# Kernel optimization log

Measured on AMD Instinct MI355X. Metric: run time of the kernel, lower is better.

The kernel has to match this reference:

```python
import jax, jax.numpy as jnp
from jax import lax
import numpy as np


def setup_inputs() -> dict:
    key = jax.random.key(0)
    ks = jax.random.split(key, 8)
    B, Cin, H, W = 4, 64, 128, 128
    D, N = 2 * Cin, 64  # D = in_ch*2, N = ssd_state_dim*2
    s = np.float32(1.0 / np.sqrt(D))
    return {
        "x": jax.random.normal(ks[0], (B, Cin, H, W), jnp.float32),
        "h_prev": jnp.zeros((B, D, N), jnp.float32),
        "norm_w": jnp.ones((D,), jnp.float32),
        "norm_b": jnp.zeros((D,), jnp.float32),
        "W_x": jax.random.normal(ks[1], (D, D), jnp.float32) * s,
        "W_B": jax.random.normal(ks[2], (N, D), jnp.float32) * s,
        "W_C": jax.random.normal(ks[3], (N, D), jnp.float32) * s,
        "w_dt": jax.random.normal(ks[4], (D,), jnp.float32) * s,
        "dt_bias": jnp.float32(0.0),
        "A_log": jnp.float32(0.0),
        "D_skip": jax.random.normal(ks[5], (D,), jnp.float32),
        "W_out": jax.random.normal(ks[6], (D, D), jnp.float32) * s,
    }


def _forward(x, h_prev, norm_w, norm_b, W_x, W_B, W_C, w_dt, dt_bias, A_log, D_skip, W_out):
    B, C, H, W = x.shape
    # rfft2 -> complex [B, C, Hf, Wf]
    xf = jnp.fft.rfft2(x, norm='ortho')
    Hf, Wf = xf.shape[-2], xf.shape[-1]
    L = Hf * Wf
    sqrt_n = jnp.sqrt(jnp.float32(H * W))
    # pack real/imag along channels: [B, 2C, L]
    u = jnp.concatenate([xf.real.reshape(B, C, L), xf.imag.reshape(B, C, L)], axis=1)
    # LayerNorm1D over the channel dim
    mu = jnp.mean(u, axis=1, keepdims=True)
    var = jnp.var(u, axis=1, keepdims=True)
    u = (u - mu) * lax.rsqrt(var + 1e-5) * norm_w[None, :, None] + norm_b[None, :, None]
    u = u / sqrt_n
    # SSD (Mamba2-style) recurrence over the L frequency tokens
    xs = jnp.einsum('ed,bdl->lbe', W_x, u)   # [L, B, D]
    Bs = jnp.einsum('nd,bdl->lbn', W_B, u)   # [L, B, N]
    Cs = jnp.einsum('nd,bdl->lbn', W_C, u)   # [L, B, N]
    dt = jax.nn.softplus(jnp.einsum('d,bdl->lb', w_dt, u) + dt_bias)  # [L, B]
    dec = jnp.exp(-jnp.exp(A_log) * dt)       # [L, B], A = -exp(A_log)

    def step(h, inp):
        x_t, B_t, C_t, dec_t, dt_t = inp
        h = dec_t[:, None, None] * h + (dt_t[:, None] * x_t)[:, :, None] * B_t[:, None, :]
        y_t = jnp.einsum('bdn,bn->bd', h, C_t)
        return h, y_t

    h_last, ys = lax.scan(step, h_prev, (xs, Bs, Cs, dec, dt))  # ys [L, B, D]
    y = ys.transpose(1, 2, 0) + D_skip[None, :, None] * xs.transpose(1, 2, 0)  # [B, D, L]
    freq_out = jnp.einsum('ed,bdl->bel', W_out, y) * sqrt_n
    # unpack real/imag halves and inverse FFT
    ft = (freq_out[:, :C] + 1j * freq_out[:, C:]).reshape(B, C, Hf, Wf)
    y_sp = jnp.fft.irfft2(ft, s=(H, W), norm='ortho')
    return y_sp, h_last


def reference(x, h_prev, norm_w, norm_b, W_x, W_B, W_C, w_dt, dt_bias, A_log, D_skip, W_out):
    return _forward(x, h_prev, norm_w, norm_b, W_x, W_B, W_C, w_dt, dt_bias, A_log, D_skip, W_out)
```

## Files before the change

kernel.cpp:

```cpp
#include <hip/hip_runtime.h>
#include <hip/hip_bf16.h>
#include <math.h>

#define BB 4
#define CC 64
#define HH 128
#define WW 128
#define DD 128
#define NN 64
#define HF 128
#define WF 65
#define LL 8320
#define TSEG 64
#define NSEG 130
#define PI2f 6.283185307179586f

__device__ __forceinline__ int brev7(int x) { return (int)(__brev((unsigned)x) >> 25); }

__global__ void k0_transpose(const float* __restrict__ Wx, const float* __restrict__ Wb,
                             const float* __restrict__ Wc, const float* __restrict__ Wout,
                             float* __restrict__ WcatT, float* __restrict__ WoT) {
  int idx = blockIdx.x * 256 + threadIdx.x;
  if (idx < 128 * 256) {
    int k = idx >> 8, o = idx & 255;
    float v;
    if (o < 128)      v = Wx[o * 128 + k];
    else if (o < 192) v = Wb[(o - 128) * 128 + k];
    else              v = Wc[(o - 192) * 128 + k];
    WcatT[k * 256 + o] = v;
  }
  if (idx < 128 * 128) {
    int d = idx >> 7, e = idx & 127;
    WoT[d * 128 + e] = Wout[e * 128 + d];
  }
}

__global__ __launch_bounds__(256) void k1_rfft(const float* __restrict__ x,
                                               float* __restrict__ T1) {
  __shared__ float2 data[128 * 17];
  __shared__ float2 tw[64];
  int tid = threadIdx.x;
  if (tid < 64) {
    float sv, cv;
    sincosf(PI2f * (float)tid * (1.f / 128.f), &sv, &cv);
    tw[tid] = make_float2(cv, sv);
  }
  int r0 = blockIdx.x * 32;
  const float* xp = x + (size_t)r0 * 128;
#pragma unroll
  for (int i = 0; i < 8; i++) {
    int e = i * 256 + tid;
    int p = e >> 7, j = e & 127;
    float v1 = xp[(2 * p) * 128 + j];
    float v2 = xp[(2 * p + 1) * 128 + j];
    data[brev7(j) * 17 + p] = make_float2(v1, v2);
  }
  __syncthreads();
  for (int s = 1; s <= 7; s++) {
    int half = 1 << (s - 1);
    int tsh = 7 - s;
#pragma unroll
    for (int i = 0; i < 4; i++) {
      int idx = i * 256 + tid;
      int t = idx >> 4, c = idx & 15;
      int j = t & (half - 1);
      int pos = ((t >> (s - 1)) << s) + j;
      float2 a = data[pos * 17 + c];
      float2 b = data[(pos + half) * 17 + c];
      float2 w = tw[j << tsh];
      float2 m = make_float2(b.x * w.x + b.y * w.y, b.y * w.x - b.x * w.y);
      data[pos * 17 + c] = make_float2(a.x + m.x, a.y + m.y);
      data[(pos + half) * 17 + c] = make_float2(a.x - m.x, a.y - m.y);
    }
    __syncthreads();
  }
  const float inv = 1.f / 128.f;
  float2* o = (float2*)T1 + (size_t)r0 * 65;
#pragma unroll
  for (int i = 0; i < 5; i++) {
    int e = i * 256 + tid;
    if (e < 1040) {
      int p = e / 65, k = e - p * 65;
      float2 Z = data[k * 17 + p];
      float2 Zc = data[((128 - k) & 127) * 17 + p];
      float2 X1 = make_float2((Z.x + Zc.x) * 0.5f * inv, (Z.y - Zc.y) * 0.5f * inv);
      float2 X2 = make_float2((Z.y + Zc.y) * 0.5f * inv, (Zc.x - Z.x) * 0.5f * inv);
      o[(2 * p) * 65 + k] = X1;
      o[(2 * p + 1) * 65 + k] = X2;
    }
  }
}

__global__ __launch_bounds__(256) void k2a_fft(const float* __restrict__ T1,
                                               float* __restrict__ uT) {
  __shared__ float2 data[128 * 34];
  __shared__ float2 tw[64];
  int tid = threadIdx.x;
  if (tid < 64) {
    float sv, cv;
    sincosf(PI2f * (float)tid * (1.f / 128.f), &sv, &cv);
    tw[tid] = make_float2(cv, sv);
  }
  int chunk = blockIdx.x & 1;
  int bc = blockIdx.x >> 1;
  int wf0 = chunk * 32;
  const float2* Tp = (const float2*)T1 + (size_t)bc * 8320;
#pragma unroll
  for (int i = 0; i < 17; i++) {
    int e = i * 256 + tid;
    if (e < 4224) {
      int j = e / 33;
      int c = e - j * 33;
      data[brev7(j) * 34 + c] = Tp[j * 65 + wf0 + c];
    }
  }
  __syncthreads();
  for (int s = 1; s <= 7; s++) {
    int half = 1 << (s - 1);
    int tsh = 7 - s;
#pragma unroll
    for (int i = 0; i < 9; i++) {
      int idx = i * 256 + tid;
      if (idx < 2112) {
        int t = idx / 33;
        int c = idx - t * 33;
        int j = t & (half - 1);
        int pos = ((t >> (s - 1)) << s) + j;
        float2 a = data[pos * 34 + c];
        float2 b = data[(pos + half) * 34 + c];
        float2 w = tw[j << tsh];
        float2 m = make_float2(b.x * w.x + b.y * w.y, b.y * w.x - b.x * w.y);
        data[pos * 34 + c] = make_float2(a.x + m.x, a.y + m.y);
        data[(pos + half) * 34 + c] = make_float2(a.x - m.x, a.y - m.y);
      }
    }
    __syncthreads();
  }
  int b = bc >> 6, ch = bc & 63;
  float* pr = uT + (size_t)(b * 128 + ch) * 8320;
  float* pi = uT + (size_t)(b * 128 + 64 + ch) * 8320;
#pragma unroll
  for (int i = 0; i < 17; i++) {
    int e = i * 256 + tid;
    if (e < 4224) {
      int hf = e / 33;
      int c = e - hf * 33;
      float2 v = data[hf * 34 + c];
      pr[hf * 65 + wf0 + c] = v.x;
      pi[hf * 65 + wf0 + c] = v.y;
    }
  }
}

__global__ __launch_bounds__(512) void k3_ln_proj(
    const float* __restrict__ uT, const float* __restrict__ WcatT,
    const float* __restrict__ nw, const float* __restrict__ nb,
    const float* __restrict__ wdt, const float* __restrict__ dtbias,
    float* __restrict__ xs, float* __restrict__ Bs, float* __restrict__ Cs,
    float* __restrict__ dtb) {
  __shared__ float su[128 * 68];
  __shared__ float snw[128], snb[128], swdt[128];
  int tid = threadIdx.x;
  int b = blockIdx.x / 130, tile = blockIdx.x % 130;
  int l0 = tile * 64;
  if (tid < 128) { snw[tid] = nw[tid]; snb[tid] = nb[tid]; swdt[tid] = wdt[tid]; }
  const float* up = uT + (size_t)b * 128 * 8320 + l0;
#pragma unroll
  for (int i = 0; i < 4; i++) {
    int e = i * 512 + tid;
    int d = e >> 4, q = e & 15;
    float4 v = *(const float4*)(up + (size_t)d * 8320 + q * 4);
    *(float4*)&su[d * 68 + q * 4] = v;
  }
  __syncthreads();
  int t = tid >> 3, j = tid & 7;
  float vals[16];
  float s = 0.f, s2 = 0.f;
#pragma unroll
  for (int i = 0; i < 16; i++) {
    float v = su[(8 * i + j) * 68 + t];
    vals[i] = v; s += v; s2 += v * v;
  }
  s += __shfl_xor(s, 1, 64);  s += __shfl_xor(s, 2, 64);  s += __shfl_xor(s, 4, 64);
  s2 += __shfl_xor(s2, 1, 64); s2 += __shfl_xor(s2, 2, 64); s2 += __shfl_xor(s2, 4, 64);
  float mu = s * (1.f / 128.f);
  float var = s2 * (1.f / 128.f) - mu * mu;
  float rs = rsqrtf(var + 1e-5f);
  float raw = 0.f;
#pragma unroll
  for (int i = 0; i < 16; i++) {
    int k = 8 * i + j;
    float v = ((vals[i] - mu) * rs * snw[k] + snb[k]) * (1.f / 128.f);
    su[k * 68 + t] = v;
    raw = fmaf(v, swdt[k], raw);
  }
  raw += __shfl_xor(raw, 1, 64); raw += __shfl_xor(raw, 2, 64); raw += __shfl_xor(raw, 4, 64);
  if (j == 0) {
    float z = raw + dtbias[0];
    float sp = fmaxf(z, 0.f) + log1pf(expf(-fabsf(z)));
    dtb[b * LL + l0 + t] = sp;
  }
  __syncthreads();
  int wv = tid >> 6;
  int lane = tid & 63;
  int t0 = wv * 8;
  float acc[8][4];
#pragma unroll
  for (int i = 0; i < 8; i++)
#pragma unroll
    for (int r = 0; r < 4; r++) acc[i][r] = 0.f;
  const float4* W4 = (const float4*)WcatT;
  for (int k = 0; k < 128; k++) {
    float4 w = W4[k * 64 + lane];
    const float4* sr4 = (const float4*)&su[k * 68 + t0];
    float4 u0 = sr4[0], u1 = sr4[1];
    float uk[8] = {u0.x, u0.y, u0.z, u0.w, u1.x, u1.y, u1.z, u1.w};
#pragma unroll
    for (int i = 0; i < 8; i++) {
      acc[i][0] = fmaf(w.x, uk[i], acc[i][0]);
      acc[i][1] = fmaf(w.y, uk[i], acc[i][1]);
      acc[i][2] = fmaf(w.z, uk[i], acc[i][2]);
      acc[i][3] = fmaf(w.w, uk[i], acc[i][3]);
    }
  }
  size_t tok0 = (size_t)b * LL + l0 + t0;
  float* basep;
  size_t stride;
  if (lane < 32)      { basep = xs + tok0 * 128 + lane * 4;        stride = 128; }
  else if (lane < 48) { basep = Bs + tok0 * 64 + (lane - 32) * 4;  stride = 64; }
  else                { basep = Cs + tok0 * 64 + (lane - 48) * 4;  stride = 64; }
#pragma unroll
  for (int i = 0; i < 8; i++)
    *(float4*)(basep + (size_t)i * stride) =
        make_float4(acc[i][0], acc[i][1], acc[i][2], acc[i][3]);
}

__global__ __launch_bounds__(256) void k5_seg(
    const float* __restrict__ xs, const float* __restrict__ Bs, const float* __restrict__ Cs,
    const float* __restrict__ dtb, const float* __restrict__ Alog,
    const float* __restrict__ Dskip,
    float* __restrict__ ybuf, float* __restrict__ Sseg, float* __restrict__ ssegb,
    float* __restrict__ cumg) {
  __shared__ __align__(16) float sX[64 * 68];
  __shared__ __align__(16) float sB[64 * 68];
  __shared__ __align__(16) float sCM[64 * 68];
  __shared__ float sdt[64], slc[64], sws[64];
  int tid = threadIdx.x;
  int half = blockIdx.x & 1;
  int bs = blockIdx.x >> 1;
  int b = bs / NSEG, seg = bs % NSEG;
  int tokbase = b * LL + seg * TSEG;
  const float4* xg = (const float4*)(xs + (size_t)tokbase * 128);
#pragma unroll
  for (int i = 0; i < 4; i++) {
    int e = i * 256 + tid;
    int t = e >> 4, q = e & 15;
    *(float4*)&sX[t * 68 + q * 4] = xg[t * 32 + half * 16 + q];
  }
  const float4* bg = (const float4*)(Bs + (size_t)tokbase * 64);
  const float4* cg = (const float4*)(Cs + (size_t)tokbase * 64);
#pragma unroll
  for (int i = 0; i < 4; i++) {
    int e = i * 256 + tid;
    int t = e >> 4, n4 = e & 15;
    *(float4*)&sB[t * 68 + n4 * 4] = bg[e];
    *(float4*)&sCM[t * 68 + n4 * 4] = cg[e];
  }
  if (tid < 64) sdt[tid] = dtb[tokbase + tid];
  __syncthreads();
  if (tid < 64) {
    float a = expf(Alog[0]);
    float v = -a * sdt[tid];
#pragma unroll
    for (int off = 1; off < 64; off <<= 1) {
      float o = __shfl_up(v, off, 64);
      if (tid >= off) v += o;
    }
    slc[tid] = v;
    float l63 = __shfl(v, 63, 64);
    sws[tid] = expf(l63 - v) * sdt[tid];
    if (half == 0) {
      cumg[tokbase + tid] = expf(v);
      if (tid == 63) ssegb[seg * BB + b] = expf(v);
    }
  }
  __syncthreads();
  int t0 = (tid >> 4) * 4, s0 = (tid & 15) * 4;
  float g[4][4];
#pragma unroll
  for (int i = 0; i < 4; i++)
#pragma unroll
    for (int j = 0; j < 4; j++) g[i][j] = 0.f;
  for (int n4 = 0; n4 < 16; n4++) {
    float4 cr[4], br[4];
#pragma unroll
    for (int i = 0; i < 4; i++) cr[i] = *(const float4*)&sCM[(t0 + i) * 68 + n4 * 4];
#pragma unroll
    for (int j = 0; j < 4; j++) br[j] = *(const float4*)&sB[(s0 + j) * 68 + n4 * 4];
#pragma unroll
    for (int i = 0; i < 4; i++)
#pragma unroll
      for (int j = 0; j < 4; j++) {
        g[i][j] = fmaf(cr[i].x, br[j].x, g[i][j]);
        g[i][j] = fmaf(cr[i].y, br[j].y, g[i][j]);
        g[i][j] = fmaf(cr[i].z, br[j].z, g[i][j]);
        g[i][j] = fmaf(cr[i].w, br[j].w, g[i][j]);
      }
  }
  __syncthreads();
#pragma unroll
  for (int i = 0; i < 4; i++) {
    int t = t0 + i;
    float4 m;
    float lt = slc[t];
    m.x = (s0 + 0 <= t) ? expf(lt - slc[s0 + 0]) * sdt[s0 + 0] * g[i][0] : 0.f;
    m.y = (s0 + 1 <= t) ? expf(lt - slc[s0 + 1]) * sdt[s0 + 1] * g[i][1] : 0.f;
    m.z = (s0 + 2 <= t) ? expf(lt - slc[s0 + 2]) * sdt[s0 + 2] * g[i][2] : 0.f;
    m.w = (s0 + 3 <= t) ? expf(lt - slc[s0 + 3]) * sdt[s0 + 3] * g[i][3] : 0.f;
    *(float4*)&sCM[t * 68 + s0] = m;
  }
  __syncthreads();
  {
    int d0 = (tid & 15) * 4;
    float acc[4][4];
#pragma unroll
    for (int i = 0; i < 4; i++)
#pragma unroll
      for (int j = 0; j < 4; j++) acc[i][j] = 0.f;
    for (int s = 0; s < 64; s++) {
      float4 xv = *(const float4*)&sX[s * 68 + d0];
#pragma unroll
      for (int i = 0; i < 4; i++) {
        float m = sCM[(t0 + i) * 68 + s];
        acc[i][0] = fmaf(m, xv.x, acc[i][0]);
        acc[i][1] = fmaf(m, xv.y, acc[i][1]);
        acc[i][2] = fmaf(m, xv.z, acc[i][2]);
        acc[i][3] = fmaf(m, xv.w, acc[i][3]);
      }
    }
    float4 dk = *(const float4*)&Dskip[half * 64 + d0];
#pragma unroll
    for (int i = 0; i < 4; i++) {
      int t = t0 + i;
      float4 xv = *(const float4*)&sX[t * 68 + d0];
      float4 y;
      y.x = fmaf(dk.x, xv.x, acc[i][0]);
      y.y = fmaf(dk.y, xv.y, acc[i][1]);
      y.z = fmaf(dk.z, xv.z, acc[i][2]);
      y.w = fmaf(dk.w, xv.w, acc[i][3]);
      *(float4*)(ybuf + (size_t)(tokbase + t) * 128 + half * 64 + d0) = y;
    }
  }
  {
    int dd0 = (tid >> 4) * 4, n0 = (tid & 15) * 4;
    float sacc[4][4];
#pragma unroll
    for (int k = 0; k < 4; k++)
#pragma unroll
      for (int j = 0; j < 4; j++) sacc[k][j] = 0.f;
    for (int s = 0; s < 64; s++) {
      float w = sws[s];
      float4 b4 = *(const float4*)&sB[s * 68 + n0];
      b4.x *= w; b4.y *= w; b4.z *= w; b4.w *= w;
      float4 xv = *(const float4*)&sX[s * 68 + dd0];
      float xk[4] = {xv.x, xv.y, xv.z, xv.w};
#pragma unroll
      for (int k = 0; k < 4; k++) {
        sacc[k][0] = fmaf(xk[k], b4.x, sacc[k][0]);
        sacc[k][1] = fmaf(xk[k], b4.y, sacc[k][1]);
        sacc[k][2] = fmaf(xk[k], b4.z, sacc[k][2]);
        sacc[k][3] = fmaf(xk[k], b4.w, sacc[k][3]);
      }
    }
    float* Sp = Sseg + (size_t)seg * 32768 + (size_t)b * 8192;
#pragma unroll
    for (int k = 0; k < 4; k++)
      *(float4*)&Sp[(half * 64 + dd0 + k) * 64 + n0] =
          make_float4(sacc[k][0], sacc[k][1], sacc[k][2], sacc[k][3]);
  }
}

__global__ void k5b_states(const float* __restrict__ h_prev, const float* __restrict__ Sseg,
                           const float* __restrict__ ssegb, float* __restrict__ Hp,
                           float* __restrict__ h_last) {
  int gid = blockIdx.x * 256 + threadIdx.x;
  int b = gid >> 13;
  float h = h_prev[gid];
  for (int p = 0; p < NSEG; p++) {
    Hp[(size_t)p * 32768 + gid] = h;
    h = fmaf(ssegb[p * 4 + b], h, Sseg[(size_t)p * 32768 + gid]);
  }
  h_last[gid] = h;
}

__global__ __launch_bounds__(512) void k5c_correct(
    const float* __restrict__ Cs, const float* __restrict__ Hp,
    const float* __restrict__ cumg, float* __restrict__ ybuf) {
  __shared__ __align__(16) float Ct[64 * 64];
  __shared__ __align__(16) float Ht[64 * 132];
  __shared__ float cg[64];
  int tid = threadIdx.x;
  int b = blockIdx.x / NSEG, seg = blockIdx.x % NSEG;
  int tokbase = b * LL + seg * 64;
  const float* Csrc = Cs + (size_t)tokbase * 64;
#pragma unroll
  for (int i = 0; i < 8; i++) {
    int e = tid + i * 512;
    Ct[(e & 63) * 64 + (e >> 6)] = Csrc[e];
  }
  const float* Hsrc = Hp + (size_t)seg * 32768 + (size_t)b * 8192;
#pragma unroll
  for (int i = 0; i < 16; i++) {
    int e = tid + i * 512;
    Ht[(e & 63) * 132 + (e >> 6)] = Hsrc[e];
  }
  if (tid < 64) cg[tid] = cumg[tokbase + tid];
  __syncthreads();
  int og = tid & 15, tg = tid >> 4;
  int d0 = og * 8, t0 = tg * 2;
  float acc[2][8];
#pragma unroll
  for (int i = 0; i < 2; i++)
#pragma unroll
    for (int jj = 0; jj < 8; jj++) acc[i][jj] = 0.f;
  for (int n = 0; n < 64; n++) {
    float2 c2 = *(const float2*)&Ct[n * 64 + t0];
    float4 h0 = *(const float4*)&Ht[n * 132 + d0];
    float4 h1 = *(const float4*)&Ht[n * 132 + d0 + 4];
    float cv[2] = {c2.x, c2.y};
    float hv[8] = {h0.x, h0.y, h0.z, h0.w, h1.x, h1.y, h1.z, h1.w};
#pragma unroll
    for (int i = 0; i < 2; i++)
#pragma unroll
      for (int jj = 0; jj < 8; jj++) acc[i][jj] = fmaf(cv[i], hv[jj], acc[i][jj]);
  }
#pragma unroll
  for (int i = 0; i < 2; i++) {
    float sc = cg[t0 + i];
    float* yp = ybuf + (size_t)(tokbase + t0 + i) * 128 + d0;
    float4 y0 = *(float4*)yp;
    float4 y1 = *(float4*)(yp + 4);
    y0.x = fmaf(sc, acc[i][0], y0.x); y0.y = fmaf(sc, acc[i][1], y0.y);
    y0.z = fmaf(sc, acc[i][2], y0.z); y0.w = fmaf(sc, acc[i][3], y0.w);
    y1.x = fmaf(sc, acc[i][4], y1.x); y1.y = fmaf(sc, acc[i][5], y1.y);
    y1.z = fmaf(sc, acc[i][6], y1.z); y1.w = fmaf(sc, acc[i][7], y1.w);
    *(float4*)yp = y0; *(float4*)(yp + 4) = y1;
  }
}

__global__ __launch_bounds__(512) void k6_outproj(
    const float* __restrict__ ybuf, const float* __restrict__ WoT,
    float* __restrict__ T2) {
  __shared__ float sy[128 * 68];
  int tid = threadIdx.x;
  int b = blockIdx.x / 130, tile = blockIdx.x % 130;
  int l0 = tile * 64;
  const float* yg = ybuf + ((size_t)b * LL + l0) * 128;
#pragma unroll
  for (int i = 0; i < 4; i++) {
    int e = i * 512 + tid;
    int t = e >> 5, q = e & 31;
    float4 v = *(const float4*)(yg + t * 128 + q * 4);
    sy[(q * 4 + 0) * 68 + t] = v.x; sy[(q * 4 + 1) * 68 + t] = v.y;
    sy[(q * 4 + 2) * 68 + t] = v.z; sy[(q * 4 + 3) * 68 + t] = v.w;
  }
  __syncthreads();
  int wv = tid >> 6;
  int lane = tid & 63;
  int o4 = lane & 31, th = lane >> 5;
  int tt0 = wv * 8 + th * 4;
  float acc[4][4];
#pragma unroll
  for (int i = 0; i < 4; i++)
#pragma unroll
    for (int r = 0; r < 4; r++) acc[i][r] = 0.f;
  const float4* W4 = (const float4*)WoT;
  for (int k = 0; k < 128; k++) {
    float4 w = W4[k * 32 + o4];
    const float4* sr4 = (const float4*)&sy[k * 68 + tt0];
    float4 u0 = sr4[0];
    float yk[4] = {u0.x, u0.y, u0.z, u0.w};
#pragma unroll
    for (int i = 0; i < 4; i++) {
      acc[i][0] = fmaf(w.x, yk[i], acc[i][0]);
      acc[i][1] = fmaf(w.y, yk[i], acc[i][1]);
      acc[i][2] = fmaf(w.z, yk[i], acc[i][2]);
      acc[i][3] = fmaf(w.w, yk[i], acc[i][3]);
    }
  }
#pragma unroll
  for (int i = 0; i < 4; i++) {
    int l = l0 + tt0 + i;
    *(float4*)(T2 + ((size_t)b * LL + l) * 128 + o4 * 4) =
        make_float4(acc[i][0] * 128.f, acc[i][1] * 128.f,
                    acc[i][2] * 128.f, acc[i][3] * 128.f);
  }
}

__global__ __launch_bounds__(256) void k7t_transpose(const float* __restrict__ T2,
                                                     float* __restrict__ T2T) {
  __shared__ __align__(16) float tile[32][132];
  int tid = threadIdx.x;
  int b = blockIdx.x / 260, lt = blockIdx.x % 260;
  int l0 = lt * 32;
#pragma unroll
  for (int i = 0; i < 4; i++) {
    int e = i * 256 + tid;
    int l = e >> 5, f4 = e & 31;
    float4 v = *(const float4*)(T2 + ((size_t)(b * LL + l0 + l)) * 128 + f4 * 4);
    *(float4*)&tile[l][f4 * 4] = v;
  }
  __syncthreads();
  int l = tid & 31, c2 = tid >> 5;
  float2* out = (float2*)T2T;
#pragma unroll
  for (int k = 0; k < 8; k++) {
    int c = c2 * 8 + k;
    float2 z = make_float2(tile[l][c], tile[l][64 + c]);
    out[((size_t)(b * 64 + c)) * 8320 + l0 + l] = z;
  }
}

__global__ __launch_bounds__(256) void k7a_fft(const float* __restrict__ T2T,
                                               float* __restrict__ TY) {
  __shared__ float2 data[128 * 34];
  __shared__ float2 tw[64];
  int tid = threadIdx.x;
  if (tid < 64) {
    float sv, cv;
    sincosf(PI2f * (float)tid * (1.f / 128.f), &sv, &cv);
    tw[tid] = make_float2(cv, sv);
  }
  int chunk = blockIdx.x & 1;
  int bc = blockIdx.x >> 1;
  int wf0 = chunk * 32;
  const float2* Zp = (const float2*)T2T + (size_t)bc * 8320;
#pragma unroll
  for (int i = 0; i < 17; i++) {
    int e = i * 256 + tid;
    if (e < 4224) {
      int j = e / 33;
      int c = e - j * 33;
      data[brev7(j) * 34 + c] = Zp[j * 65 + wf0 + c];
    }
  }
  __syncthreads();
  for (int s = 1; s <= 7; s++) {
    int half = 1 << (s - 1);
    int tsh = 7 - s;
#pragma unroll
    for (int i = 0; i < 9; i++) {
      int idx = i * 256 + tid;
      if (idx < 2112) {
        int t = idx / 33;
        int c = idx - t * 33;
        int j = t & (half - 1);
        int pos = ((t >> (s - 1)) << s) + j;
        float2 a = data[pos * 34 + c];
        float2 b = data[(pos + half) * 34 + c];
        float2 w = tw[j << tsh];
        float2 m = make_float2(b.x * w.x - b.y * w.y, b.y * w.x + b.x * w.y);
        data[pos * 34 + c] = make_float2(a.x + m.x, a.y + m.y);
        data[(pos + half) * 34 + c] = make_float2(a.x - m.x, a.y - m.y);
      }
    }
    __syncthreads();
  }
  float2* po = (float2*)TY + (size_t)bc * 8320;
#pragma unroll
  for (int i = 0; i < 17; i++) {
    int e = i * 256 + tid;
    if (e < 4224) {
      int h = e / 33;
      int c = e - h * 33;
      po[h * 65 + wf0 + c] = data[h * 34 + c];
    }
  }
}

__global__ __launch_bounds__(256) void k8_irfft(const float* __restrict__ TY,
                                                float* __restrict__ out) {
  __shared__ float2 zsh[32 * 66];
  __shared__ float2 data[128 * 17];
  __shared__ float2 tw[64];
  int tid = threadIdx.x;
  if (tid < 64) {
    float sv, cv;
    sincosf(PI2f * (float)tid * (1.f / 128.f), &sv, &cv);
    tw[tid] = make_float2(cv, sv);
  }
  int r0 = blockIdx.x * 32;
  const float2* Zp = (const float2*)TY + (size_t)r0 * 65;
#pragma unroll
  for (int i = 0; i < 9; i++) {
    int e = i * 256 + tid;
    if (e < 2080) {
      int r = e / 65, wf = e - r * 65;
      zsh[r * 66 + wf] = Zp[r * 65 + wf];
    }
  }
  __syncthreads();
#pragma unroll
  for (int i = 0; i < 8; i++) {
    int e = i * 256 + tid;
    int p = e >> 7, j = e & 127;
    int jj = (j <= 64) ? j : 128 - j;
    float2 a1 = zsh[(2 * p) * 66 + jj];
    float2 a2 = zsh[(2 * p + 1) * 66 + jj];
    if (jj == 0 || jj == 64) { a1.y = 0.f; a2.y = 0.f; }
    float2 V = (j <= 64) ? make_float2(a1.x - a2.y, a1.y + a2.x)
                         : make_float2(a1.x + a2.y, a2.x - a1.y);
    data[brev7(j) * 17 + p] = V;
  }
  __syncthreads();
  for (int s = 1; s <= 7; s++) {
    int half = 1 << (s - 1);
    int tsh = 7 - s;
#pragma unroll
    for (int i = 0; i < 4; i++) {
      int idx = i * 256 + tid;
      int t = idx >> 4, c = idx & 15;
      int j = t & (half - 1);
      int pos = ((t >> (s - 1)) << s) + j;
      float2 a = data[pos * 17 + c];
      float2 b = data[(pos + half) * 17 + c];
      float2 w = tw[j << tsh];
      float2 m = make_float2(b.x * w.x - b.y * w.y, b.y * w.x + b.x * w.y);
      data[pos * 17 + c] = make_float2(a.x + m.x, a.y + m.y);
      data[(pos + half) * 17 + c] = make_float2(a.x - m.x, a.y - m.y);
    }
    __syncthreads();
  }
  const float inv = 1.f / 128.f;
  float* op = out + (size_t)r0 * 128;
#pragma unroll
  for (int i = 0; i < 8; i++) {
    int e = i * 256 + tid;
    int p = e >> 7, w = e & 127;
    float2 X = data[w * 17 + p];
    op[(2 * p) * 128 + w] = X.x * inv;
    op[(2 * p + 1) * 128 + w] = X.y * inv;
  }
}

extern "C" void kernel_launch(void* const* d_in, const int* in_sizes, int n_in,
                              void* d_out, int out_size, void* d_ws, size_t ws_size,
                              hipStream_t stream) {
  const float* x      = (const float*)d_in[0];
  const float* h_prev = (const float*)d_in[1];
  const float* nw     = (const float*)d_in[2];
  const float* nb     = (const float*)d_in[3];
  const float* Wx     = (const float*)d_in[4];
  const float* Wb     = (const float*)d_in[5];
  const float* Wc     = (const float*)d_in[6];
  const float* wdt    = (const float*)d_in[7];
  const float* dtbias = (const float*)d_in[8];
  const float* Alog   = (const float*)d_in[9];
  const float* Dskip  = (const float*)d_in[10];
  const float* Wout   = (const float*)d_in[11];
  float* out = (float*)d_out;

  float* ws = (float*)d_ws;
  const size_t SZ_BIG = 4259840;
  const size_t SZ_BN  = 2129920;
  float* RA = ws;
  float* RB = RA + SZ_BIG;
  float* RC = RB + SZ_BIG;
  float* RD = RC + SZ_BIG;
  float* RE = RD + SZ_BN;
  float* dtb   = RE + SZ_BN;
  float* cumg  = dtb + 33280;
  float* ssegb = cumg + 33280;
  float* WcatT = ssegb + 520;
  float* WoT   = WcatT + 32768;

  hipLaunchKernelGGL(k0_transpose, dim3(128), dim3(256), 0, stream, Wx, Wb, Wc, Wout, WcatT, WoT);
  hipLaunchKernelGGL(k1_rfft, dim3(1024), dim3(256), 0, stream, x, RA );
  hipLaunchKernelGGL(k2a_fft, dim3(512), dim3(256), 0, stream, RA , RB );
  hipLaunchKernelGGL(k3_ln_proj, dim3(520), dim3(512), 0, stream,
                     RB , WcatT, nw, nb, wdt, dtbias, RA , RD , RE , dtb);
  hipLaunchKernelGGL(k5_seg, dim3(1040), dim3(256), 0, stream,
                     RA , RD , RE , dtb, Alog, Dskip,
                     RB , RC , ssegb, cumg);
  hipLaunchKernelGGL(k5b_states, dim3(128), dim3(256), 0, stream,
                     h_prev, RC , ssegb, RA , out + 4194304);
  hipLaunchKernelGGL(k5c_correct, dim3(520), dim3(512), 0, stream,
                     RE , RA , cumg, RB );
  hipLaunchKernelGGL(k6_outproj, dim3(520), dim3(512), 0, stream, RB , WoT, RC );
  hipLaunchKernelGGL(k7t_transpose, dim3(1040), dim3(256), 0, stream, RC , RD );
  hipLaunchKernelGGL(k7a_fft, dim3(512), dim3(256), 0, stream, RD , RA );
  hipLaunchKernelGGL(k8_irfft, dim3(1024), dim3(256), 0, stream, RA , out);
}
```

Baseline: 218.0 us.

## Merge k5_seg half-blocks and read x tiles from global instead of LDS

k5_seg now runs one block per (batch, segment) covering all 128 channels instead of two blocks that each handle half. The C·B Gram matrix, decay cumsum and B loads are no longer computed twice. The sX shared-memory staging is removed and x values are read directly from global (L1/L2 cached) inside the inner loops. Each thread's tile doubles to 8 columns, which raises register pressure and leaves half as many blocks, and the per-iteration global loads may cost more latency than LDS reads.

```diff
diff --git a/kernel.cpp b/kernel.cpp
--- a/kernel.cpp
+++ b/kernel.cpp
@@ -241,22 +241,13 @@
     const float* __restrict__ Dskip,
     float* __restrict__ ybuf, float* __restrict__ Sseg, float* __restrict__ ssegb,
     float* __restrict__ cumg) {
-  __shared__ __align__(16) float sX[64 * 68];
   __shared__ __align__(16) float sB[64 * 68];
   __shared__ __align__(16) float sCM[64 * 68];
   __shared__ float sdt[64], slc[64], sws[64];
   int tid = threadIdx.x;
-  int half = blockIdx.x & 1;
-  int bs = blockIdx.x >> 1;
-  int b = bs / NSEG, seg = bs % NSEG;
+  int b = blockIdx.x / NSEG, seg = blockIdx.x % NSEG;
   int tokbase = b * LL + seg * TSEG;
   const float4* xg = (const float4*)(xs + (size_t)tokbase * 128);
-#pragma unroll
-  for (int i = 0; i < 4; i++) {
-    int e = i * 256 + tid;
-    int t = e >> 4, q = e & 15;
-    *(float4*)&sX[t * 68 + q * 4] = xg[t * 32 + half * 16 + q];
-  }
   const float4* bg = (const float4*)(Bs + (size_t)tokbase * 64);
   const float4* cg = (const float4*)(Cs + (size_t)tokbase * 64);
 #pragma unroll
@@ -279,10 +270,8 @@
     slc[tid] = v;
     float l63 = __shfl(v, 63, 64);
     sws[tid] = expf(l63 - v) * sdt[tid];
-    if (half == 0) {
-      cumg[tokbase + tid] = expf(v);
-      if (tid == 63) ssegb[seg * BB + b] = expf(v);
-    }
+    cumg[tokbase + tid] = expf(v);
+    if (tid == 63) ssegb[seg * BB + b] = expf(v);
   }
   __syncthreads();
   int t0 = (tid >> 4) * 4, s0 = (tid & 15) * 4;
@@ -321,61 +310,70 @@
   }
   __syncthreads();
   {
-    int d0 = (tid & 15) * 4;
-    float acc[4][4];
+    int d4 = (tid & 15) * 2;
+    float acc[4][8];
 #pragma unroll
     for (int i = 0; i < 4; i++)
 #pragma unroll
-      for (int j = 0; j < 4; j++) acc[i][j] = 0.f;
+      for (int j = 0; j < 8; j++) acc[i][j] = 0.f;
     for (int s = 0; s < 64; s++) {
-      float4 xv = *(const float4*)&sX[s * 68 + d0];
+      float4 x0 = xg[s * 32 + d4];
+      float4 x1 = xg[s * 32 + d4 + 1];
+      float xv[8] = {x0.x, x0.y, x0.z, x0.w, x1.x, x1.y, x1.z, x1.w};
 #pragma unroll
       for (int i = 0; i < 4; i++) {
         float m = sCM[(t0 + i) * 68 + s];
-        acc[i][0] = fmaf(m, xv.x, acc[i][0]);
-        acc[i][1] = fmaf(m, xv.y, acc[i][1]);
-        acc[i][2] = fmaf(m, xv.z, acc[i][2]);
-        acc[i][3] = fmaf(m, xv.w, acc[i][3]);
+#pragma unroll
+        for (int j = 0; j < 8; j++) acc[i][j] = fmaf(m, xv[j], acc[i][j]);
       }
     }
-    float4 dk = *(const float4*)&Dskip[half * 64 + d0];
+    int d0 = d4 * 4;
+    float4 dk0 = *(const float4*)&Dskip[d0];
+    float4 dk1 = *(const float4*)&Dskip[d0 + 4];
+    float dk[8] = {dk0.x, dk0.y, dk0.z, dk0.w, dk1.x, dk1.y, dk1.z, dk1.w};
 #pragma unroll
     for (int i = 0; i < 4; i++) {
       int t = t0 + i;
-      float4 xv = *(const float4*)&sX[t * 68 + d0];
-      float4 y;
-      y.x = fmaf(dk.x, xv.x, acc[i][0]);
-      y.y = fmaf(dk.y, xv.y, acc[i][1]);
-      y.z = fmaf(dk.z, xv.z, acc[i][2]);
-      y.w = fmaf(dk.w, xv.w, acc[i][3]);
-      *(float4*)(ybuf + (size_t)(tokbase + t) * 128 + half * 64 + d0) = y;
+      float4 x0 = xg[t * 32 + d4];
+      float4 x1 = xg[t * 32 + d4 + 1];
+      float xv[8] = {x0.x, x0.y, x0.z, x0.w, x1.x, x1.y, x1.z, x1.w};
+      float4 y0, y1;
+      y0.x = fmaf(dk[0], xv[0], acc[i][0]); y0.y = fmaf(dk[1], xv[1], acc[i][1]);
+      y0.z = fmaf(dk[2], xv[2], acc[i][2]); y0.w = fmaf(dk[3], xv[3], acc[i][3]);
+      y1.x = fmaf(dk[4], xv[4], acc[i][4]); y1.y = fmaf(dk[5], xv[5], acc[i][5]);
+      y1.z = fmaf(dk[6], xv[6], acc[i][6]); y1.w = fmaf(dk[7], xv[7], acc[i][7]);
+      float* yp = ybuf + (size_t)(tokbase + t) * 128 + d0;
+      *(float4*)yp = y0;
+      *(float4*)(yp + 4) = y1;
     }
   }
   {
-    int dd0 = (tid >> 4) * 4, n0 = (tid & 15) * 4;
-    float sacc[4][4];
-#pragma unroll
-    for (int k = 0; k < 4; k++)
+    int dd4 = (tid >> 4) * 2, n0 = (tid & 15) * 4;
+    float sacc[8][4];
+#pragma unroll
+    for (int k = 0; k < 8; k++)
 #pragma unroll
       for (int j = 0; j < 4; j++) sacc[k][j] = 0.f;
     for (int s = 0; s < 64; s++) {
       float w = sws[s];
       float4 b4 = *(const float4*)&sB[s * 68 + n0];
       b4.x *= w; b4.y *= w; b4.z *= w; b4.w *= w;
-      float4 xv = *(const float4*)&sX[s * 68 + dd0];
-      float xk[4] = {xv.x, xv.y, xv.z, xv.w};
-#pragma unroll
-      for (int k = 0; k < 4; k++) {
-        sacc[k][0] = fmaf(xk[k], b4.x, sacc[k][0]);
-        sacc[k][1] = fmaf(xk[k], b4.y, sacc[k][1]);
-        sacc[k][2] = fmaf(xk[k], b4.z, sacc[k][2]);
-        sacc[k][3] = fmaf(xk[k], b4.w, sacc[k][3]);
+      float4 x0 = xg[s * 32 + dd4];
+      float4 x1 = xg[s * 32 + dd4 + 1];
+      float xv[8] = {x0.x, x0.y, x0.z, x0.w, x1.x, x1.y, x1.z, x1.w};
+#pragma unroll
+      for (int k = 0; k < 8; k++) {
+        sacc[k][0] = fmaf(xv[k], b4.x, sacc[k][0]);
+        sacc[k][1] = fmaf(xv[k], b4.y, sacc[k][1]);
+        sacc[k][2] = fmaf(xv[k], b4.z, sacc[k][2]);
+        sacc[k][3] = fmaf(xv[k], b4.w, sacc[k][3]);
       }
     }
+    int dd0 = dd4 * 4;
     float* Sp = Sseg + (size_t)seg * 32768 + (size_t)b * 8192;
 #pragma unroll
-    for (int k = 0; k < 4; k++)
-      *(float4*)&Sp[(half * 64 + dd0 + k) * 64 + n0] =
+    for (int k = 0; k < 8; k++)
+      *(float4*)&Sp[(dd0 + k) * 64 + n0] =
           make_float4(sacc[k][0], sacc[k][1], sacc[k][2], sacc[k][3]);
   }
 }
@@ -679,7 +677,7 @@
   hipLaunchKernelGGL(k2a_fft, dim3(512), dim3(256), 0, stream, RA , RB );
   hipLaunchKernelGGL(k3_ln_proj, dim3(520), dim3(512), 0, stream,
                      RB , WcatT, nw, nb, wdt, dtbias, RA , RD , RE , dtb);
-  hipLaunchKernelGGL(k5_seg, dim3(1040), dim3(256), 0, stream,
+  hipLaunchKernelGGL(k5_seg, dim3(520), dim3(256), 0, stream,
                      RA , RD , RE , dtb, Alog, Dskip,
                      RB , RC , ssegb, cumg);
   hipLaunchKernelGGL(k5b_states, dim3(128), dim3(256), 0, stream,
```

Measured after the change: 218.4 us. Within noise of the previous version (+0.2%).
